# Optimization experiments

Hardware: AMD Instinct MI355X
Metric: run time of the kernel (lower is better)

The kernel has to match this reference:

```python
import jax, jax.numpy as jnp
import numpy as np

B, T, D, H, W = 4, 16, 64, 64, 64
EXPAND = 4
D2 = 2 * D


def _ln(x, g, b, eps=1e-5):
    m = jnp.mean(x, axis=-1, keepdims=True)
    v = jnp.var(x, axis=-1, keepdims=True)
    return (x - m) * jax.lax.rsqrt(v + eps) * g + b


def _cnorm(z, g, b):
    # complex LayerNorm: LN over concatenated [real, imag] last dim
    zc = jnp.concatenate([z.real, z.imag], axis=-1)
    zn = _ln(zc, g, b)
    r, i = jnp.split(zn, 2, axis=-1)
    return r + 1j * i


def setup_inputs() -> dict:
    key = jax.random.key(0)
    ks = jax.random.split(key, 16)
    sD = 1.0 / np.sqrt(D)
    return {
        "x_real": jax.random.normal(ks[0], (B, T, D, H, W), jnp.float32),
        "x_imag": jax.random.normal(ks[1], (B, T, D, H, W), jnp.float32),
        "dt": jax.random.uniform(ks[2], (B,), jnp.float32, 0.5, 1.5),
        "ln_s_g": jnp.ones((D2,), jnp.float32),
        "ln_s_b": jnp.zeros((D2,), jnp.float32),
        "conv_w": jax.random.normal(ks[3], (D2, D2, 3, 3), jnp.float32) * 0.02,
        "conv_b": jnp.zeros((D2,), jnp.float32),
        "spec_wr": jax.random.normal(ks[4], (D, H, W), jnp.float32) * 0.1,
        "spec_wi": jax.random.normal(ks[5], (D, H, W), jnp.float32) * 0.1,
        "gate": jnp.full((1,), 0.5, jnp.float32),
        "ln_t_g": jnp.ones((D2,), jnp.float32),
        "ln_t_b": jnp.zeros((D2,), jnp.float32),
        "lam_r": -jnp.abs(jax.random.normal(ks[6], (D,), jnp.float32)) * 0.1 - 0.01,
        "lam_i": jax.random.normal(ks[7], (D,), jnp.float32) * 0.5,
        "enc_r": jax.random.normal(ks[8], (D, D), jnp.float32) * sD,
        "enc_i": jax.random.normal(ks[9], (D, D), jnp.float32) * sD,
        "dec_r": jax.random.normal(ks[10], (D, D), jnp.float32) * sD,
        "dec_i": jax.random.normal(ks[11], (D, D), jnp.float32) * sD,
        "p_w1": jax.random.normal(ks[12], (D2, D2 * EXPAND), jnp.float32) * 0.02,
        "p_b1": jnp.zeros((D2 * EXPAND,), jnp.float32),
        "p_w2": jax.random.normal(ks[13], (D2 * EXPAND, D2), jnp.float32) * 0.02,
        "p_b2": jnp.zeros((D2,), jnp.float32),
    }


def reference(x_real, x_imag, dt, ln_s_g, ln_s_b, conv_w, conv_b, spec_wr,
              spec_wi, gate, ln_t_g, ln_t_b, lam_r, lam_i, enc_r, enc_i,
              dec_r, dec_i, p_w1, p_b1, p_w2, p_b2):
    x = x_real + 1j * x_imag                                   # (B,T,D,H,W) c64
    # ---- spatial branch ----
    resid = x
    x_s = jnp.transpose(x.reshape(B * T, D, H, W), (0, 2, 3, 1))   # (BT,H,W,D)
    x_s = jnp.transpose(_cnorm(x_s, ln_s_g, ln_s_b), (0, 3, 1, 2)) # (BT,D,H,W)
    xri = jnp.concatenate([x_s.real, x_s.imag], axis=1)            # (BT,2D,H,W)
    oc = jax.lax.conv_general_dilated(
        xri, conv_w, (1, 1), 'SAME',
        dimension_numbers=('NCHW', 'OIHW', 'NCHW')) + conv_b[None, :, None, None]
    r, i = jnp.split(oc, 2, axis=1)
    cliff = r + 1j * i
    spec_w = spec_wr + 1j * spec_wi                                # (D,H,W)
    spec = jnp.fft.ifft2(jnp.fft.fft2(x_s, axes=(-2, -1)) * spec_w[None],
                         axes=(-2, -1))
    x_s = gate[0] * cliff + (1.0 - gate[0]) * spec
    x = x_s.reshape(B, T, D, H, W) + resid
    # ---- temporal branch: diagonal linear recurrence ----
    resid = x
    x_t = jnp.transpose(x, (0, 3, 4, 1, 2)).reshape(B, H * W, T, D)
    x_t = _cnorm(x_t, ln_t_g, ln_t_b)
    lam = lam_r + 1j * lam_i                                       # (D,)
    decay = jnp.exp(lam[None, :] * dt[:, None])                    # (B,D) c64
    forcing = (decay - 1.0) / lam[None, :]                         # ZOH input op
    E = enc_r + 1j * enc_i
    Dm = dec_r + 1j * dec_i
    x_eigen = jnp.einsum('bntd,de->bnte', x_t, E)                  # (B,HW,T,D)

    def step(h, u):                                                # h:(B,HW,D)
        h = h * decay[:, None, :] + u * forcing[:, None, :]
        return h, h

    h0 = jnp.zeros((B, H * W, D), jnp.complex64)
    _, h_eig = jax.lax.scan(step, h0, jnp.moveaxis(x_eigen, 2, 0))
    h_eig = jnp.moveaxis(h_eig, 0, 2)                              # (B,HW,T,D)
    dec = jnp.einsum('bntd,de->bnte', h_eig, Dm)
    x_drift = jnp.transpose(dec.real.reshape(B, H, W, T, D), (0, 3, 4, 1, 2))
    x = x_drift + resid
    # ---- para-pool channel MLP ----
    resid = x
    x_p = jnp.transpose(x, (0, 1, 3, 4, 2))                        # (B,T,H,W,D)
    xpf = jnp.concatenate([x_p.real, x_p.imag], axis=-1)           # (B,T,H,W,2D)
    h1 = jax.nn.gelu(jnp.einsum('bthwc,cf->bthwf', xpf, p_w1) + p_b1)
    h2 = jnp.einsum('bthwf,fc->bthwc', h1, p_w2) + p_b2
    r, i = jnp.split(h2, 2, axis=-1)
    x = jnp.transpose(r + 1j * i, (0, 1, 4, 2, 3)) + resid
    # return real representation: concat real/imag on channel axis
    return jnp.concatenate([x.real, x.imag], axis=2)               # (B,T,2D,H,W)
```

## Files before the change

kernel.cpp:

```cpp
#include <hip/hip_runtime.h>
#include <hip/hip_bf16.h>

#define NB 4
#define NT 16
#define ND 64
#define NHW 4096
#define NTOT (NB*NT*ND*NHW)

typedef __attribute__((ext_vector_type(8))) __bf16 bf16x8;
typedef __attribute__((ext_vector_type(4))) __bf16 bf16x4;
typedef __attribute__((ext_vector_type(4))) float f32x4;

__global__ void k_ln(const float* __restrict__ xr, const float* __restrict__ xi,
                     const float* __restrict__ g, const float* __restrict__ b,
                     float* __restrict__ outr, float* __restrict__ outi) {
  int pos = blockIdx.x * 256 + threadIdx.x;
  int bt = pos >> 12;
  int hw = pos & 4095;
  size_t base = (size_t)bt * ND * NHW + hw;
  float s = 0.f, ss = 0.f;
  for (int d = 0; d < ND; ++d) {
    float r = xr[base + (size_t)d * NHW];
    float im = xi[base + (size_t)d * NHW];
    s += r + im; ss += r * r + im * im;
  }
  float mean = s * (1.0f / 128.0f);
  float var = ss * (1.0f / 128.0f) - mean * mean;
  float rstd = rsqrtf(var + 1e-5f);
  for (int d = 0; d < ND; ++d) {
    float r = xr[base + (size_t)d * NHW];
    float im = xi[base + (size_t)d * NHW];
    outr[base + (size_t)d * NHW] = (r - mean) * rstd * g[d] + b[d];
    outi[base + (size_t)d * NHW] = (im - mean) * rstd * g[64 + d] + b[64 + d];
  }
}

__global__ void k_wconv_repack(const float* __restrict__ w, __hip_bfloat16* __restrict__ wcp) {
  int idx = blockIdx.x * 256 + threadIdx.x;
  int j = idx & 7;
  int lane = (idx >> 3) & 63;
  int kt = (idx >> 9) & 3;
  int nt = (idx >> 11) & 7;
  int tap = idx >> 14;
  int ic = kt * 32 + (lane >> 4) * 8 + j;
  int oc = nt * 16 + (lane & 15);
  wcp[idx] = __float2bfloat16(w[((size_t)(oc * 128 + ic)) * 9 + tap]);
}

__global__ __launch_bounds__(256) void k_conv_mfma(
    const float* __restrict__ xsr, const float* __restrict__ xsi,
    const __hip_bfloat16* __restrict__ wcp, const float* __restrict__ bias,
    __hip_bfloat16* __restrict__ cr, __hip_bfloat16* __restrict__ ci) {
  __shared__ __align__(16) __bf16 lin[3 * 66 * 128];
  int blk = blockIdx.x;
  int y = blk & 63;
  int bt = blk >> 6;
  int tid = threadIdx.x;
  int lane = tid & 63, wave = tid >> 6;
  int lc = lane & 15, quad = lane >> 4;

  for (int i = tid; i < 48 * 66; i += 256) {
    int p = i / 66;
    int pos = i - p * 66;
    int ky = p >> 4, icg = p & 15;
    int gy = y + ky - 1, gx = pos - 1;
    float vals[8];
#pragma unroll
    for (int k = 0; k < 8; ++k) vals[k] = 0.f;
    if (gy >= 0 && gy < 64 && gx >= 0 && gx < 64) {
      const float* src = (icg < 8) ? xsr : xsi;
      size_t pbase = ((size_t)(bt * 64 + (icg & 7) * 8)) * NHW + gy * 64 + gx;
#pragma unroll
      for (int k = 0; k < 8; ++k) vals[k] = src[pbase + (size_t)k * NHW];
    }
    bf16x8 v;
#pragma unroll
    for (int k = 0; k < 8; ++k) v[k] = (__bf16)vals[k];
    int elem = ((ky * 66 + pos) * 128 + icg * 8) ^ ((pos & 7) << 3);
    *(bf16x8*)(lin + elem) = v;
  }
  __syncthreads();

  int mt0 = (wave >> 1) * 2;
  int ocb = (wave & 1) * 4;
  f32x4 acc[2][4];
#pragma unroll
  for (int m = 0; m < 2; ++m)
#pragma unroll
    for (int n = 0; n < 4; ++n) acc[m][n] = (f32x4){0.f, 0.f, 0.f, 0.f};

  for (int ky = 0; ky < 3; ++ky) {
#pragma unroll
    for (int kt = 0; kt < 4; ++kt) {
      bf16x8 a[3][2];
#pragma unroll
      for (int kx = 0; kx < 3; ++kx)
#pragma unroll
        for (int m = 0; m < 2; ++m) {
          int pos = (mt0 + m) * 16 + lc + kx;
          int elem = ((ky * 66 + pos) * 128 + kt * 32 + quad * 8) ^ ((pos & 7) << 3);
          a[kx][m] = *(const bf16x8*)(lin + elem);
        }
#pragma unroll
      for (int kx = 0; kx < 3; ++kx) {
        const __hip_bfloat16* wp =
            wcp + ((((size_t)(ky * 3 + kx) * 8 + ocb) * 4 + kt) * 64 + lane) * 8;
#pragma unroll
        for (int n = 0; n < 4; ++n) {
          bf16x8 b = *(const bf16x8*)(const void*)(wp + (size_t)n * (4 * 64 * 8));
#pragma unroll
          for (int m = 0; m < 2; ++m)
            acc[m][n] = __builtin_amdgcn_mfma_f32_16x16x32_bf16(a[kx][m], b, acc[m][n], 0, 0, 0);
        }
      }
    }
  }
  __syncthreads();

  __bf16* lout = lin;
#pragma unroll
  for (int n = 0; n < 4; ++n) {
    int oc = (ocb + n) * 16 + lc;
    float bb = bias[oc];
#pragma unroll
    for (int m = 0; m < 2; ++m)
#pragma unroll
      for (int r = 0; r < 4; ++r)
        lout[oc * 66 + (mt0 + m) * 16 + quad * 4 + r] = (__bf16)(acc[m][n][r] + bb);
  }
  __syncthreads();

  {
    int colh = (lane & 31) * 2;
    int ocl = lane >> 5;
#pragma unroll
    for (int it = 0; it < 16; ++it) {
      int oc = it * 8 + wave * 2 + ocl;
      __hip_bfloat16* dst = (oc < 64) ? cr : ci;
      size_t ob = ((size_t)(bt * 64 + (oc & 63))) * NHW + y * 64 + colh;
      *(unsigned int*)((void*)(dst + ob)) =
          *(const unsigned int*)((const void*)(lout + oc * 66 + colh));
    }
  }
}

__device__ __forceinline__ void gemm64x128(const __bf16* __restrict__ src,
                                           const __hip_bfloat16* __restrict__ bp,
                                           int lane, int lc, int quad, int w,
                                           f32x4 (&acc)[4][2]) {
#pragma unroll
  for (int m = 0; m < 4; ++m)
#pragma unroll
    for (int n = 0; n < 2; ++n) acc[m][n] = (f32x4){0.f, 0.f, 0.f, 0.f};
#pragma unroll
  for (int kt = 0; kt < 4; ++kt) {
    bf16x8 a[4];
#pragma unroll
    for (int m = 0; m < 4; ++m)
      a[m] = *(const bf16x8*)&src[(m * 16 + lc) * 136 + kt * 32 + quad * 8];
#pragma unroll
    for (int n = 0; n < 2; ++n) {
      int ntg = w + n * 4;
      bf16x8 b = *(const bf16x8*)(const void*)(bp + (((size_t)ntg * 4 + kt) * 64 + lane) * 8);
#pragma unroll
      for (int m = 0; m < 4; ++m)
        acc[m][n] = __builtin_amdgcn_mfma_f32_16x16x32_bf16(a[m], b, acc[m][n], 0, 0, 0);
    }
  }
}
__device__ __forceinline__ void store_T(__bf16* __restrict__ dst,
                                        int lc, int quad, int w, f32x4 (&acc)[4][2]) {
#pragma unroll
  for (int m = 0; m < 4; ++m)
#pragma unroll
    for (int n = 0; n < 2; ++n) {
      bf16x4 v;
#pragma unroll
      for (int r = 0; r < 4; ++r) v[r] = (__bf16)acc[m][n][r];
      *(bf16x4*)&dst[(w * 16 + lc) * 136 + n * 64 + m * 16 + quad * 4] = v;
    }
}

__global__ __launch_bounds__(256) void k_fft_mfma(
    float* xsr, float* xsi,
    const __hip_bfloat16* __restrict__ cr, const __hip_bfloat16* __restrict__ ci,
    const float* __restrict__ swr, const float* __restrict__ swi,
    const float* __restrict__ x0r, const float* __restrict__ x0i,
    const float* __restrict__ gate,
    const __hip_bfloat16* __restrict__ Fp, const __hip_bfloat16* __restrict__ Gp) {
  __shared__ __align__(16) __bf16 lA[64 * 136];
  __shared__ __align__(16) __bf16 lB[64 * 136];
  int slice = blockIdx.x;
  int d = slice & 63;
  size_t base = (size_t)slice * NHW;
  int tid = threadIdx.x, lane = tid & 63, w = tid >> 6;
  int lc = lane & 15, quad = lane >> 4;
  float g = gate[0];

  {
    int y = tid >> 2, xo = (tid & 3) * 4;
#pragma unroll
    for (int k = 0; k < 4; ++k) {
      int x = xo + k * 16;
      float4 vr = *(const float4*)(xsr + base + y * 64 + x);
      float4 vi = *(const float4*)(xsi + base + y * 64 + x);
      bf16x4 br_, bi_;
#pragma unroll
      for (int r = 0; r < 4; ++r) { br_[r] = (__bf16)(&vr.x)[r]; bi_[r] = (__bf16)(&vi.x)[r]; }
      *(bf16x4*)&lA[y * 136 + x] = br_;
      *(bf16x4*)&lA[y * 136 + 64 + x] = bi_;
    }
  }
  __syncthreads();
  f32x4 acc[4][2];
  gemm64x128(lA, Fp, lane, lc, quad, w, acc);
  store_T(lB, lc, quad, w, acc);
  __syncthreads();
  gemm64x128(lB, Fp, lane, lc, quad, w, acc);
  {
    int ky = w * 16 + lc;
    const float* wrp = swr + (size_t)d * 4096 + ky * 64;
    const float* wip = swi + (size_t)d * 4096 + ky * 64;
#pragma unroll
    for (int m = 0; m < 4; ++m) {
      int kx0 = m * 16 + quad * 4;
      float4 wr4 = *(const float4*)(wrp + kx0);
      float4 wi4 = *(const float4*)(wip + kx0);
      bf16x4 zr4, zi4;
#pragma unroll
      for (int r = 0; r < 4; ++r) {
        float yr = acc[m][0][r], yi = acc[m][1][r];
        float wr = (&wr4.x)[r], wi = (&wi4.x)[r];
        zr4[r] = (__bf16)(yr * wr - yi * wi);
        zi4[r] = (__bf16)(yr * wi + yi * wr);
      }
      *(bf16x4*)&lA[ky * 136 + kx0] = zr4;
      *(bf16x4*)&lA[ky * 136 + 64 + kx0] = zi4;
    }
  }
  __syncthreads();
  gemm64x128(lA, Gp, lane, lc, quad, w, acc);
  store_T(lB, lc, quad, w, acc);
  __syncthreads();
  gemm64x128(lB, Gp, lane, lc, quad, w, acc);
  {
    int y = w * 16 + lc;
#pragma unroll
    for (int m = 0; m < 4; ++m) {
      int x = m * 16 + quad * 4;
      size_t off = base + y * 64 + x;
      float4 v0r = *(const float4*)(x0r + off);
      float4 v0i = *(const float4*)(x0i + off);
      bf16x4 c4r = *(const bf16x4*)((const __bf16*)cr + off);
      bf16x4 c4i = *(const bf16x4*)((const __bf16*)ci + off);
      float4 outr, outi;
#pragma unroll
      for (int r = 0; r < 4; ++r) {
        (&outr.x)[r] = g * (float)c4r[r] + (1.f - g) * acc[m][0][r] + (&v0r.x)[r];
        (&outi.x)[r] = g * (float)c4i[r] + (1.f - g) * acc[m][1][r] + (&v0i.x)[r];
      }
      *(float4*)(xsr + off) = outr;
      *(float4*)(xsi + off) = outi;
    }
  }
}

__global__ void k_repack_all(const float* __restrict__ w1, const float* __restrict__ w2,
                             const float* __restrict__ er, const float* __restrict__ ei,
                             const float* __restrict__ dmr, const float* __restrict__ dmi,
                             __hip_bfloat16* __restrict__ w1p, __hip_bfloat16* __restrict__ w2p,
                             __hip_bfloat16* __restrict__ encp, __hip_bfloat16* __restrict__ decp,
                             __hip_bfloat16* __restrict__ fp, __hip_bfloat16* __restrict__ gp) {
  int idx = blockIdx.x * 256 + threadIdx.x;
  if (idx < 65536) {
    int j = idx & 7, lane = (idx >> 3) & 63, kt = (idx >> 9) & 3, nt = idx >> 11;
    int k = kt * 32 + (lane >> 4) * 8 + j;
    int n = nt * 16 + (lane & 15);
    w1p[idx] = __float2bfloat16(w1[k * 512 + n]);
  } else if (idx < 131072) {
    int i2 = idx - 65536;
    int j = i2 & 7, lane = (i2 >> 3) & 63, kt = (i2 >> 9) & 15, nt = i2 >> 13;
    int k = kt * 32 + (lane >> 4) * 8 + j;
    int n = nt * 16 + (lane & 15);
    w2p[i2] = __float2bfloat16(w2[k * 128 + n]);
  } else if (idx < 147456) {
    int i2 = idx - 131072;
    int j = i2 & 7, lane = (i2 >> 3) & 63, kt = (i2 >> 9) & 3, nt = i2 >> 11;
    int k = kt * 32 + (lane >> 4) * 8 + j;
    int n = nt * 16 + (lane & 15);
    float v;
    if (k < 64) v = (n < 64) ? er[k * 64 + n] : ei[k * 64 + (n - 64)];
    else        v = (n < 64) ? -ei[(k - 64) * 64 + n] : er[(k - 64) * 64 + (n - 64)];
    encp[i2] = __float2bfloat16(v);
  } else if (idx < 155648) {
    int i2 = idx - 147456;
    int j = i2 & 7, lane = (i2 >> 3) & 63, kt = (i2 >> 9) & 3, nt = i2 >> 11;
    int k = kt * 32 + (lane >> 4) * 8 + j;
    int n = nt * 16 + (lane & 15);
    float v = (k < 64) ? dmr[k * 64 + n] : -dmi[(k - 64) * 64 + n];
    decp[i2] = __float2bfloat16(v);
  } else if (idx < 172032) {
    int i2 = idx - 155648;
    int j = i2 & 7, lane = (i2 >> 3) & 63, kt = (i2 >> 9) & 3, nt = i2 >> 11;
    int k = kt * 32 + (lane >> 4) * 8 + j;
    int n = nt * 16 + (lane & 15);
    int p = ((k & 63) * (n & 63)) & 63;
    float sv, cv;
    __sincosf((float)p * 0.09817477042f, &sv, &cv);
    float v = ((k < 64) == (n < 64)) ? cv : ((n >= 64) ? -sv : sv);
    fp[i2] = __float2bfloat16(v);
  } else {
    int i2 = idx - 172032;
    int j = i2 & 7, lane = (i2 >> 3) & 63, kt = (i2 >> 9) & 3, nt = i2 >> 11;
    int k = kt * 32 + (lane >> 4) * 8 + j;
    int n = nt * 16 + (lane & 15);
    int p = ((k & 63) * (n & 63)) & 63;
    float sv, cv;
    __sincosf((float)p * 0.09817477042f, &sv, &cv);
    float v = (((k < 64) == (n < 64)) ? cv : ((n >= 64) ? sv : -sv)) * 0.015625f;
    gp[i2] = __float2bfloat16(v);
  }
}

__global__ __launch_bounds__(256) void k_ln_enc(
    const float* __restrict__ xsr, const float* __restrict__ xsi,
    const float* __restrict__ lng, const float* __restrict__ lnb,
    const __hip_bfloat16* __restrict__ encp,
    __hip_bfloat16* __restrict__ xer, __hip_bfloat16* __restrict__ xei) {
  __shared__ __bf16 la[32 * 136];
  __shared__ float red_s[8][33], red_ss[8][33];
  int blk = blockIdx.x;
  int bt = blk >> 7;
  int hw0 = (blk & 127) << 5;
  int tid = threadIdx.x;
  int lane = tid & 63, wave = tid >> 6;
  int lc = lane & 15, quad = lane >> 4;
  int tok = tid & 31, cg = tid >> 5;
  float v[16];
  float s = 0.f, ss = 0.f;
#pragma unroll
  for (int it = 0; it < 16; ++it) {
    int c = it * 8 + cg;
    const float* src = (c < 64) ? (xsr + ((size_t)(bt * 64 + c)) * NHW)
                                : (xsi + ((size_t)(bt * 64 + c - 64)) * NHW);
    v[it] = src[hw0 + tok];
    s += v[it]; ss += v[it] * v[it];
  }
  red_s[cg][tok] = s; red_ss[cg][tok] = ss;
  __syncthreads();
  float S = 0.f, SS = 0.f;
#pragma unroll
  for (int k = 0; k < 8; ++k) { S += red_s[k][tok]; SS += red_ss[k][tok]; }
  float mean = S * (1.0f / 128.0f);
  float rstd = rsqrtf(SS * (1.0f / 128.0f) - mean * mean + 1e-5f);
#pragma unroll
  for (int it = 0; it < 16; ++it) {
    int c = it * 8 + cg;
    la[tok * 136 + c] = (__bf16)((v[it] - mean) * rstd * lng[c] + lnb[c]);
  }
  __syncthreads();
  f32x4 acc[2][2];
#pragma unroll
  for (int m = 0; m < 2; ++m)
#pragma unroll
    for (int n = 0; n < 2; ++n) acc[m][n] = (f32x4){0.f, 0.f, 0.f, 0.f};
#pragma unroll
  for (int kt = 0; kt < 4; ++kt) {
    bf16x8 a0 = *(const bf16x8*)&la[lc * 136 + kt * 32 + quad * 8];
    bf16x8 a1 = *(const bf16x8*)&la[(lc + 16) * 136 + kt * 32 + quad * 8];
#pragma unroll
    for (int n = 0; n < 2; ++n) {
      int ntg = wave * 2 + n;
      bf16x8 b = *(const bf16x8*)(const void*)(encp + (((size_t)ntg * 4 + kt) * 64 + lane) * 8);
      acc[0][n] = __builtin_amdgcn_mfma_f32_16x16x32_bf16(a0, b, acc[0][n], 0, 0, 0);
      acc[1][n] = __builtin_amdgcn_mfma_f32_16x16x32_bf16(a1, b, acc[1][n], 0, 0, 0);
    }
  }
  __syncthreads();
  __bf16* lo = la;
#pragma unroll
  for (int n = 0; n < 2; ++n) {
    int c = (wave * 2 + n) * 16 + lc;
#pragma unroll
    for (int m = 0; m < 2; ++m)
#pragma unroll
      for (int r = 0; r < 4; ++r)
        lo[c * 34 + m * 16 + quad * 4 + r] = (__bf16)acc[m][n][r];
  }
  __syncthreads();
  {
    int tokh = tid & 15, cc = tid >> 4;
#pragma unroll
    for (int it = 0; it < 8; ++it) {
      int c = it * 16 + cc;
      __hip_bfloat16* dst = (c < 64) ? xer : xei;
      size_t ob = ((size_t)(bt * 64 + (c & 63))) * NHW + hw0 + tokh * 2;
      *(unsigned int*)((void*)(dst + ob)) =
          *(const unsigned int*)((const void*)(lo + c * 34 + tokh * 2));
    }
  }
}

__global__ __launch_bounds__(256) void k_scan(
    __hip_bfloat16* xer, __hip_bfloat16* xei,
    const float* __restrict__ lam_r, const float* __restrict__ lam_i,
    const float* __restrict__ dtv) {
  int idx = blockIdx.x * 256 + threadIdx.x;
  int hw = idx & 4095;
  int e = (idx >> 12) & 63;
  int b = idx >> 18;
  float lrv = lam_r[e], liv = lam_i[e];
  float dtb = dtv[b];
  float mg = __expf(lrv * dtb);
  float sn, cs;
  __sincosf(liv * dtb, &sn, &cs);
  float der = mg * cs, dei = mg * sn;
  float nr = der - 1.0f, ni = dei;
  float dn = 1.0f / (lrv * lrv + liv * liv);
  float forr = (nr * lrv + ni * liv) * dn;
  float fori = (ni * lrv - nr * liv) * dn;
  float hr = 0.f, hi = 0.f;
  size_t base = ((size_t)(b * NT * ND + e)) * NHW + hw;
  for (int t = 0; t < NT; ++t) {
    size_t off = base + (size_t)t * ND * NHW;
    float ur = __bfloat162float(xer[off]);
    float ui = __bfloat162float(xei[off]);
    float h0r = hr, h0i = hi;
    hr = h0r * der - h0i * dei + ur * forr - ui * fori;
    hi = h0r * dei + h0i * der + ur * fori + ui * forr;
    xer[off] = __float2bfloat16(hr);
    xei[off] = __float2bfloat16(hi);
  }
}

__global__ __launch_bounds__(256) void k_dec(
    float* __restrict__ xsr,
    const __hip_bfloat16* __restrict__ her, const __hip_bfloat16* __restrict__ hei,
    const __hip_bfloat16* __restrict__ decp) {
  __shared__ __bf16 lh2[32 * 136];
  int blk = blockIdx.x;
  int bt = blk >> 7;
  int hw0 = (blk & 127) << 5;
  int tid = threadIdx.x;
  int lane = tid & 63, wave = tid >> 6;
  int lc = lane & 15, quad = lane >> 4;
  {
    int tok = tid & 31, cg = tid >> 5;
#pragma unroll
    for (int it = 0; it < 16; ++it) {
      int c = it * 8 + cg;
      const __hip_bfloat16* src = (c < 64) ? (her + ((size_t)(bt * 64 + c)) * NHW)
                                           : (hei + ((size_t)(bt * 64 + c - 64)) * NHW);
      lh2[tok * 136 + c] = ((const __bf16*)src)[hw0 + tok];
    }
  }
  __syncthreads();
  f32x4 acc[2];
  acc[0] = (f32x4){0.f, 0.f, 0.f, 0.f};
  acc[1] = (f32x4){0.f, 0.f, 0.f, 0.f};
#pragma unroll
  for (int kt = 0; kt < 4; ++kt) {
    bf16x8 a0 = *(const bf16x8*)&lh2[lc * 136 + kt * 32 + quad * 8];
    bf16x8 a1 = *(const bf16x8*)&lh2[(lc + 16) * 136 + kt * 32 + quad * 8];
    bf16x8 b = *(const bf16x8*)(const void*)(decp + (((size_t)wave * 4 + kt) * 64 + lane) * 8);
    acc[0] = __builtin_amdgcn_mfma_f32_16x16x32_bf16(a0, b, acc[0], 0, 0, 0);
    acc[1] = __builtin_amdgcn_mfma_f32_16x16x32_bf16(a1, b, acc[1], 0, 0, 0);
  }
  __syncthreads();
  float* lo = (float*)lh2;
  {
    int c = wave * 16 + lc;
#pragma unroll
    for (int m = 0; m < 2; ++m)
#pragma unroll
      for (int r = 0; r < 4; ++r)
        lo[c * 33 + m * 16 + quad * 4 + r] = acc[m][r];
  }
  __syncthreads();
  {
    int tok = tid & 31, cg = tid >> 5;
#pragma unroll
    for (int it = 0; it < 8; ++it) {
      int c = it * 8 + cg;
      size_t off = ((size_t)(bt * 64 + c)) * NHW + hw0 + tok;
      xsr[off] += lo[c * 33 + tok];
    }
  }
}

__global__ __launch_bounds__(256, 3) void k_mlp_mfma(
    const float* __restrict__ xsr, const float* __restrict__ xsi,
    const __hip_bfloat16* __restrict__ w1p, const __hip_bfloat16* __restrict__ w2p,
    const float* __restrict__ b1, const float* __restrict__ b2,
    float* __restrict__ out) {
  __shared__ __bf16 lf[32 * 136];
  __shared__ __bf16 lh[32 * 520];
  float* lo = (float*)lh;
  int blk = blockIdx.x;
  int bt = blk >> 7;
  int hw0 = (blk & 127) << 5;
  int tid = threadIdx.x;
  int lane = tid & 63, wave = tid >> 6;
  int lc = lane & 15, quad = lane >> 4;
  {
    int tok = tid & 31, cg = tid >> 5;
#pragma unroll
    for (int it = 0; it < 16; ++it) {
      int c = it * 8 + cg;
      const float* src = (c < 64) ? (xsr + ((size_t)(bt * 64 + c)) * NHW)
                                  : (xsi + ((size_t)(bt * 64 + c - 64)) * NHW);
      lf[tok * 136 + c] = (__bf16)src[hw0 + tok];
    }
  }
  __syncthreads();
  f32x4 acc[2][8];
#pragma unroll
  for (int mt = 0; mt < 2; ++mt)
#pragma unroll
    for (int nt = 0; nt < 8; ++nt) acc[mt][nt] = (f32x4){0.f, 0.f, 0.f, 0.f};
#pragma unroll
  for (int kt = 0; kt < 4; ++kt) {
    bf16x8 a0 = *(const bf16x8*)&lf[lc * 136 + kt * 32 + quad * 8];
    bf16x8 a1 = *(const bf16x8*)&lf[(lc + 16) * 136 + kt * 32 + quad * 8];
    const __hip_bfloat16* wp = w1p + (((size_t)(wave * 8) * 4 + kt) * 64 + lane) * 8;
#pragma unroll
    for (int nt = 0; nt < 8; ++nt) {
      bf16x8 b = *(const bf16x8*)(const void*)(wp + (size_t)nt * (4 * 64 * 8));
      acc[0][nt] = __builtin_amdgcn_mfma_f32_16x16x32_bf16(a0, b, acc[0][nt], 0, 0, 0);
      acc[1][nt] = __builtin_amdgcn_mfma_f32_16x16x32_bf16(a1, b, acc[1][nt], 0, 0, 0);
    }
  }
#pragma unroll
  for (int nt = 0; nt < 8; ++nt) {
    int col = wave * 128 + nt * 16 + lc;
    float bb = b1[col];
#pragma unroll
    for (int mt = 0; mt < 2; ++mt)
#pragma unroll
      for (int r = 0; r < 4; ++r) {
        float x = acc[mt][nt][r] + bb;
        float y = 0.7978845608f * (x + 0.044715f * x * x * x);
        float e = __expf(2.0f * y);
        float th = 1.0f - 2.0f / (e + 1.0f);
        float gv = 0.5f * x * (1.0f + th);
        lh[(mt * 16 + quad * 4 + r) * 520 + col] = (__bf16)gv;
      }
  }
  __syncthreads();
  f32x4 acc2[2][2];
#pragma unroll
  for (int mt = 0; mt < 2; ++mt)
#pragma unroll
    for (int n = 0; n < 2; ++n) acc2[mt][n] = (f32x4){0.f, 0.f, 0.f, 0.f};
#pragma unroll
  for (int kt = 0; kt < 16; ++kt) {
    bf16x8 a0 = *(const bf16x8*)&lh[lc * 520 + kt * 32 + quad * 8];
    bf16x8 a1 = *(const bf16x8*)&lh[(lc + 16) * 520 + kt * 32 + quad * 8];
#pragma unroll
    for (int n = 0; n < 2; ++n) {
      bf16x8 b = *(const bf16x8*)(const void*)(w2p + (((size_t)(wave * 2 + n) * 16 + kt) * 64 + lane) * 8);
      acc2[0][n] = __builtin_amdgcn_mfma_f32_16x16x32_bf16(a0, b, acc2[0][n], 0, 0, 0);
      acc2[1][n] = __builtin_amdgcn_mfma_f32_16x16x32_bf16(a1, b, acc2[1][n], 0, 0, 0);
    }
  }
  __syncthreads();
#pragma unroll
  for (int n = 0; n < 2; ++n) {
    int c = wave * 32 + n * 16 + lc;
    float bb = b2[c];
#pragma unroll
    for (int mt = 0; mt < 2; ++mt)
#pragma unroll
      for (int r = 0; r < 4; ++r)
        lo[c * 33 + mt * 16 + quad * 4 + r] = acc2[mt][n][r] + bb;
  }
  __syncthreads();
  {
    int tok = tid & 31, cg = tid >> 5;
#pragma unroll
    for (int it = 0; it < 16; ++it) {
      int c = it * 8 + cg;
      const float* src = (c < 64) ? (xsr + ((size_t)(bt * 64 + c)) * NHW)
                                  : (xsi + ((size_t)(bt * 64 + c - 64)) * NHW);
      out[((size_t)(bt * 128 + c)) * NHW + hw0 + tok] = lo[c * 33 + tok] + src[hw0 + tok];
    }
  }
}

extern "C" void kernel_launch(void* const* d_in, const int* in_sizes, int n_in,
                              void* d_out, int out_size, void* d_ws, size_t ws_size,
                              hipStream_t stream) {
  const float* x_r    = (const float*)d_in[0];
  const float* x_i    = (const float*)d_in[1];
  const float* dt     = (const float*)d_in[2];
  const float* ln_s_g = (const float*)d_in[3];
  const float* ln_s_b = (const float*)d_in[4];
  const float* conv_w = (const float*)d_in[5];
  const float* conv_b = (const float*)d_in[6];
  const float* spec_wr= (const float*)d_in[7];
  const float* spec_wi= (const float*)d_in[8];
  const float* gate   = (const float*)d_in[9];
  const float* ln_t_g = (const float*)d_in[10];
  const float* ln_t_b = (const float*)d_in[11];
  const float* lam_r  = (const float*)d_in[12];
  const float* lam_i  = (const float*)d_in[13];
  const float* enc_r  = (const float*)d_in[14];
  const float* enc_i  = (const float*)d_in[15];
  const float* dec_r  = (const float*)d_in[16];
  const float* dec_i  = (const float*)d_in[17];
  const float* p_w1   = (const float*)d_in[18];
  const float* p_b1   = (const float*)d_in[19];
  const float* p_w2   = (const float*)d_in[20];
  const float* p_b2   = (const float*)d_in[21];

  float* ws   = (float*)d_ws;
  float* xs_r = ws;
  float* xs_i = ws + (size_t)NTOT;
  __hip_bfloat16* sbpack = (__hip_bfloat16*)(ws + (size_t)2 * NTOT);
  __hip_bfloat16* w1p  = sbpack;
  __hip_bfloat16* w2p  = sbpack + 65536;
  __hip_bfloat16* encp = sbpack + 131072;
  __hip_bfloat16* decp = sbpack + 147456;
  __hip_bfloat16* Fp   = sbpack + 155648;
  __hip_bfloat16* Gp   = sbpack + 172032;
  __hip_bfloat16* cl_r = (__hip_bfloat16*)(ws + (size_t)2 * NTOT + (size_t)2 * ND * NHW);
  __hip_bfloat16* cl_i = cl_r + (size_t)NTOT;
  __hip_bfloat16* wcp = (__hip_bfloat16*)d_out;

  k_repack_all<<<736, 256, 0, stream>>>(p_w1, p_w2, enc_r, enc_i, dec_r, dec_i,
                                        w1p, w2p, encp, decp, Fp, Gp);
  k_wconv_repack<<<576, 256, 0, stream>>>(conv_w, wcp);
  k_ln<<<1024, 256, 0, stream>>>(x_r, x_i, ln_s_g, ln_s_b, xs_r, xs_i);
  k_conv_mfma<<<4096, 256, 0, stream>>>(xs_r, xs_i, wcp, conv_b, cl_r, cl_i);
  k_fft_mfma<<<4096, 256, 0, stream>>>(xs_r, xs_i, cl_r, cl_i, spec_wr, spec_wi,
                                       x_r, x_i, gate, Fp, Gp);
  k_ln_enc<<<8192, 256, 0, stream>>>(xs_r, xs_i, ln_t_g, ln_t_b, encp, cl_r, cl_i);
  k_scan<<<4096, 256, 0, stream>>>(cl_r, cl_i, lam_r, lam_i, dt);
  k_dec<<<8192, 256, 0, stream>>>(xs_r, cl_r, cl_i, decp);
  k_mlp_mfma<<<8192, 256, 0, stream>>>(xs_r, xs_i, w1p, w2p, p_b1, p_b2, (float*)d_out);
}
```

Before: 814.5 us.

## Retile MLP kernel to 64 tokens with 8 waves and chunked hidden dim

The channel-MLP kernel now processes 64 tokens per block with 512 threads. The hidden dimension is split into two 256-wide chunks, so the GELU intermediate buffer in LDS is halved and each weight fragment is reused across four M-tiles instead of two. Global loads and stores are vectorized to float4. GELU is rewritten as x*sigmoid using exp2 and a hardware reciprocal. The trade-offs are more barriers, higher register pressure per thread, and slightly different GELU numerics.

Result: faster. 780.7 us (-4.2%).

```diff
diff --git a/kernel.cpp b/kernel.cpp
--- a/kernel.cpp
+++ b/kernel.cpp
@@ -488,101 +488,100 @@
   }
 }
 
-__global__ __launch_bounds__(256, 3) void k_mlp_mfma(
+__global__ __launch_bounds__(512, 6) void k_mlp_mfma(
     const float* __restrict__ xsr, const float* __restrict__ xsi,
     const __hip_bfloat16* __restrict__ w1p, const __hip_bfloat16* __restrict__ w2p,
     const float* __restrict__ b1, const float* __restrict__ b2,
     float* __restrict__ out) {
-  __shared__ __bf16 lf[32 * 136];
-  __shared__ __bf16 lh[32 * 520];
+  __shared__ __align__(16) __bf16 lf[64 * 136];
+  __shared__ __align__(16) __bf16 lh[64 * 264];
   float* lo = (float*)lh;
   int blk = blockIdx.x;
-  int bt = blk >> 7;
-  int hw0 = (blk & 127) << 5;
+  int bt = blk >> 6;
+  int hw0 = (blk & 63) << 6;
   int tid = threadIdx.x;
   int lane = tid & 63, wave = tid >> 6;
   int lc = lane & 15, quad = lane >> 4;
   {
-    int tok = tid & 31, cg = tid >> 5;
-#pragma unroll
-    for (int it = 0; it < 16; ++it) {
-      int c = it * 8 + cg;
+    int tok4 = (tid & 15) * 4, cgrp = tid >> 4;
+#pragma unroll
+    for (int it = 0; it < 4; ++it) {
+      int c = it * 32 + cgrp;
       const float* src = (c < 64) ? (xsr + ((size_t)(bt * 64 + c)) * NHW)
                                   : (xsi + ((size_t)(bt * 64 + c - 64)) * NHW);
-      lf[tok * 136 + c] = (__bf16)src[hw0 + tok];
-    }
-  }
-  __syncthreads();
-  f32x4 acc[2][8];
-#pragma unroll
-  for (int mt = 0; mt < 2; ++mt)
-#pragma unroll
-    for (int nt = 0; nt < 8; ++nt) acc[mt][nt] = (f32x4){0.f, 0.f, 0.f, 0.f};
-#pragma unroll
-  for (int kt = 0; kt < 4; ++kt) {
-    bf16x8 a0 = *(const bf16x8*)&lf[lc * 136 + kt * 32 + quad * 8];
-    bf16x8 a1 = *(const bf16x8*)&lf[(lc + 16) * 136 + kt * 32 + quad * 8];
-    const __hip_bfloat16* wp = w1p + (((size_t)(wave * 8) * 4 + kt) * 64 + lane) * 8;
-#pragma unroll
-    for (int nt = 0; nt < 8; ++nt) {
-      bf16x8 b = *(const bf16x8*)(const void*)(wp + (size_t)nt * (4 * 64 * 8));
-      acc[0][nt] = __builtin_amdgcn_mfma_f32_16x16x32_bf16(a0, b, acc[0][nt], 0, 0, 0);
-      acc[1][nt] = __builtin_amdgcn_mfma_f32_16x16x32_bf16(a1, b, acc[1][nt], 0, 0, 0);
-    }
-  }
-#pragma unroll
-  for (int nt = 0; nt < 8; ++nt) {
-    int col = wave * 128 + nt * 16 + lc;
-    float bb = b1[col];
-#pragma unroll
-    for (int mt = 0; mt < 2; ++mt)
-#pragma unroll
-      for (int r = 0; r < 4; ++r) {
-        float x = acc[mt][nt][r] + bb;
-        float y = 0.7978845608f * (x + 0.044715f * x * x * x);
-        float e = __expf(2.0f * y);
-        float th = 1.0f - 2.0f / (e + 1.0f);
-        float gv = 0.5f * x * (1.0f + th);
-        lh[(mt * 16 + quad * 4 + r) * 520 + col] = (__bf16)gv;
+      float4 v = *(const float4*)(src + hw0 + tok4);
+#pragma unroll
+      for (int r = 0; r < 4; ++r) lf[(tok4 + r) * 136 + c] = (__bf16)(&v.x)[r];
+    }
+  }
+  __syncthreads();
+  f32x4 acc2[4];
+#pragma unroll
+  for (int m = 0; m < 4; ++m) acc2[m] = (f32x4){0.f, 0.f, 0.f, 0.f};
+#pragma unroll
+  for (int fb = 0; fb < 2; ++fb) {
+#pragma unroll
+    for (int n = 0; n < 2; ++n) {
+      f32x4 acc1[4];
+#pragma unroll
+      for (int m = 0; m < 4; ++m) acc1[m] = (f32x4){0.f, 0.f, 0.f, 0.f};
+      int ntg = fb * 16 + wave * 2 + n;
+#pragma unroll
+      for (int kt = 0; kt < 4; ++kt) {
+        bf16x8 b = *(const bf16x8*)(const void*)(w1p + (((size_t)ntg * 4 + kt) * 64 + lane) * 8);
+#pragma unroll
+        for (int m = 0; m < 4; ++m) {
+          bf16x8 a = *(const bf16x8*)&lf[(m * 16 + lc) * 136 + kt * 32 + quad * 8];
+          acc1[m] = __builtin_amdgcn_mfma_f32_16x16x32_bf16(a, b, acc1[m], 0, 0, 0);
+        }
       }
-  }
-  __syncthreads();
-  f32x4 acc2[2][2];
-#pragma unroll
-  for (int mt = 0; mt < 2; ++mt)
-#pragma unroll
-    for (int n = 0; n < 2; ++n) acc2[mt][n] = (f32x4){0.f, 0.f, 0.f, 0.f};
-#pragma unroll
-  for (int kt = 0; kt < 16; ++kt) {
-    bf16x8 a0 = *(const bf16x8*)&lh[lc * 520 + kt * 32 + quad * 8];
-    bf16x8 a1 = *(const bf16x8*)&lh[(lc + 16) * 520 + kt * 32 + quad * 8];
-#pragma unroll
-    for (int n = 0; n < 2; ++n) {
-      bf16x8 b = *(const bf16x8*)(const void*)(w2p + (((size_t)(wave * 2 + n) * 16 + kt) * 64 + lane) * 8);
-      acc2[0][n] = __builtin_amdgcn_mfma_f32_16x16x32_bf16(a0, b, acc2[0][n], 0, 0, 0);
-      acc2[1][n] = __builtin_amdgcn_mfma_f32_16x16x32_bf16(a1, b, acc2[1][n], 0, 0, 0);
-    }
-  }
-  __syncthreads();
-#pragma unroll
-  for (int n = 0; n < 2; ++n) {
-    int c = wave * 32 + n * 16 + lc;
+      int f_loc = (wave * 2 + n) * 16 + lc;
+      float bb = b1[fb * 256 + f_loc];
+#pragma unroll
+      for (int m = 0; m < 4; ++m)
+#pragma unroll
+        for (int r = 0; r < 4; ++r) {
+          float x = acc1[m][r] + bb;
+          float u = __builtin_fmaf(-0.1029453f, x * x, -2.3022077f);
+          float e = exp2f(x * u);
+          float gv = x * __builtin_amdgcn_rcpf(1.0f + e);
+          lh[(m * 16 + quad * 4 + r) * 264 + f_loc] = (__bf16)gv;
+        }
+    }
+    __syncthreads();
+#pragma unroll
+    for (int kt = 0; kt < 8; ++kt) {
+      bf16x8 b = *(const bf16x8*)(const void*)(w2p + (((size_t)(wave * 16 + fb * 8 + kt) * 64 + lane)) * 8);
+#pragma unroll
+      for (int m = 0; m < 4; ++m) {
+        bf16x8 a = *(const bf16x8*)&lh[(m * 16 + lc) * 264 + kt * 32 + quad * 8];
+        acc2[m] = __builtin_amdgcn_mfma_f32_16x16x32_bf16(a, b, acc2[m], 0, 0, 0);
+      }
+    }
+    __syncthreads();
+  }
+  {
+    int c = wave * 16 + lc;
     float bb = b2[c];
 #pragma unroll
-    for (int mt = 0; mt < 2; ++mt)
+    for (int m = 0; m < 4; ++m)
 #pragma unroll
       for (int r = 0; r < 4; ++r)
-        lo[c * 33 + mt * 16 + quad * 4 + r] = acc2[mt][n][r] + bb;
-  }
-  __syncthreads();
-  {
-    int tok = tid & 31, cg = tid >> 5;
-#pragma unroll
-    for (int it = 0; it < 16; ++it) {
-      int c = it * 8 + cg;
+        lo[c * 66 + m * 16 + quad * 4 + r] = acc2[m][r] + bb;
+  }
+  __syncthreads();
+  {
+    int tok4 = (tid & 15) * 4, cgrp = tid >> 4;
+#pragma unroll
+    for (int it = 0; it < 4; ++it) {
+      int c = it * 32 + cgrp;
       const float* src = (c < 64) ? (xsr + ((size_t)(bt * 64 + c)) * NHW)
                                   : (xsi + ((size_t)(bt * 64 + c - 64)) * NHW);
-      out[((size_t)(bt * 128 + c)) * NHW + hw0 + tok] = lo[c * 33 + tok] + src[hw0 + tok];
+      float4 rv = *(const float4*)(src + hw0 + tok4);
+      float4 o;
+#pragma unroll
+      for (int r = 0; r < 4; ++r) (&o.x)[r] = lo[c * 66 + tok4 + r] + (&rv.x)[r];
+      *(float4*)(out + ((size_t)(bt * 128 + c)) * NHW + hw0 + tok4) = o;
     }
   }
 }
@@ -637,5 +636,5 @@
   k_ln_enc<<<8192, 256, 0, stream>>>(xs_r, xs_i, ln_t_g, ln_t_b, encp, cl_r, cl_i);
   k_scan<<<4096, 256, 0, stream>>>(cl_r, cl_i, lam_r, lam_i, dt);
   k_dec<<<8192, 256, 0, stream>>>(xs_r, cl_r, cl_i, decp);
-  k_mlp_mfma<<<8192, 256, 0, stream>>>(xs_r, xs_i, w1p, w2p, p_b1, p_b2, (float*)d_out);
-}
+  k_mlp_mfma<<<4096, 512, 0, stream>>>(xs_r, xs_i, w1p, w2p, p_b1, p_b2, (float*)d_out);
+}
```
